# Optimization experiments

Measured on AMD Instinct MI355X. Metric: run time of the kernel, lower is better.

## Reference

```python
import jax, jax.numpy as jnp
import numpy as np

MAX_NORM = 20.0
V, D, B, L, K = 100000, 64, 4096, 50, 3


def setup_inputs() -> dict:
    key = jax.random.key(0)
    k0, k1, k2, k3 = jax.random.split(key, 4)
    embeddings = jax.random.normal(k0, (V, D), dtype=jnp.float32)
    tokens_l = jax.random.randint(k1, (B, L), 0, V)
    tokens_r = jax.random.randint(k2, (B, L), 0, V)
    tokens_neg = jax.random.randint(k3, (B, K, L), 0, V)
    return {"embeddings": embeddings, "tokens_l": tokens_l,
            "tokens_r": tokens_r, "tokens_neg": tokens_neg}


def _renorm(w):
    # nn.Embedding(max_norm=20): rows with norm > max_norm are rescaled to max_norm
    norms = jnp.linalg.norm(w, axis=1, keepdims=True)
    scale = jnp.where(norms > MAX_NORM, MAX_NORM / norms, 1.0)
    return w * scale


def _embed_bag(w, tokens):
    # gather rows then sum-pool over the last (token) axis -> embedding-bag 'sum'
    return jnp.take(w, tokens, axis=0).sum(axis=-2)


def reference(embeddings, tokens_l, tokens_r, tokens_neg):
    w = _renorm(embeddings)
    l_batch = _embed_bag(w, tokens_l)[:, None, :]     # [B, 1, D]
    r_batch = _embed_bag(w, tokens_r)[:, None, :]     # [B, 1, D]
    neg_batch = _embed_bag(w, tokens_neg)             # [B, K, D]
    return (l_batch, r_batch, neg_batch)
```

## Files before the change

### kernel.cpp

```cpp
#include <hip/hip_runtime.h>
#include <math.h>

#define V_SZ 100000
#define D_SZ 64
#define B_SZ 4096
#define L_SZ 50
#define K_SZ 3
#define MAX_NORM 20.0f

__global__ __launch_bounds__(256) void renorm_scale_kernel(
    const float* __restrict__ emb, float* __restrict__ scale) {
    int row = blockIdx.x * 16 + (threadIdx.x >> 4);
    int lane16 = threadIdx.x & 15;
    if (row >= V_SZ) return;
    const float4* row4 = (const float4*)(emb + (long)row * D_SZ);
    float4 v = row4[lane16];
    float ss = v.x * v.x + v.y * v.y + v.z * v.z + v.w * v.w;
    #pragma unroll
    for (int off = 8; off >= 1; off >>= 1)
        ss += __shfl_xor(ss, off, 16);
    if (lane16 == 0) {
        float n = sqrtf(ss);
        scale[row] = (n > MAX_NORM) ? (MAX_NORM / n) : 1.0f;
    }
}

__global__ __launch_bounds__(256) void embed_bag_kernel(
    const float* __restrict__ emb, const float* __restrict__ scale,
    const int* __restrict__ tl, const int* __restrict__ tr,
    const int* __restrict__ tn, float* __restrict__ out) {
    const int NBAGS = B_SZ * (2 + K_SZ);
    int wave = (int)((blockIdx.x * (unsigned)blockDim.x + threadIdx.x) >> 6);
    int lane = threadIdx.x & 63;
    if (wave >= NBAGS) return;

    const int* tok;
    if (wave < B_SZ)            tok = tl + (long)wave * L_SZ;
    else if (wave < 2 * B_SZ)   tok = tr + (long)(wave - B_SZ) * L_SZ;
    else                        tok = tn + (long)(wave - 2 * B_SZ) * L_SZ;

    int   t = (lane < L_SZ) ? tok[lane] : 0;
    float s = (lane < L_SZ) ? scale[t] : 0.0f;

    int m = lane & 15;
    int g = lane >> 4;

    float4 acc = make_float4(0.f, 0.f, 0.f, 0.f);
    #pragma unroll
    for (int i = 0; i < 13; ++i) {
        int j = i * 4 + g;
        int   tj = __shfl(t, j, 64);
        float sj = __shfl(s, j, 64);
        const float4* row = (const float4*)(emb + (long)tj * D_SZ);
        float4 v = row[m];
        acc.x = fmaf(sj, v.x, acc.x);
        acc.y = fmaf(sj, v.y, acc.y);
        acc.z = fmaf(sj, v.z, acc.z);
        acc.w = fmaf(sj, v.w, acc.w);
    }

    #pragma unroll
    for (int off = 16; off <= 32; off <<= 1) {
        acc.x += __shfl_xor(acc.x, off, 64);
        acc.y += __shfl_xor(acc.y, off, 64);
        acc.z += __shfl_xor(acc.z, off, 64);
        acc.w += __shfl_xor(acc.w, off, 64);
    }
    if (g == 0) {
        float4* o = (float4*)(out + (long)wave * D_SZ);
        o[m] = acc;
    }
}

extern "C" void kernel_launch(void* const* d_in, const int* in_sizes, int n_in,
                              void* d_out, int out_size, void* d_ws, size_t ws_size,
                              hipStream_t stream) {
    const float* emb = (const float*)d_in[0];
    const int* tl = (const int*)d_in[1];
    const int* tr = (const int*)d_in[2];
    const int* tn = (const int*)d_in[3];
    float* out = (float*)d_out;
    float* scale = (float*)d_ws;

    renorm_scale_kernel<<<(V_SZ + 15) / 16, 256, 0, stream>>>(emb, scale);

    const int NBAGS = B_SZ * (2 + K_SZ);
    int grid = NBAGS / 4;
    embed_bag_kernel<<<grid, 256, 0, stream>>>(emb, scale, tl, tr, tn, out);
}
```

Before: 110.7 us.

## Fuse row renorm into embedding-bag gather, drop separate scale kernel

Removes the separate kernel that computed a per-row scale over the whole vocabulary. Each gathered row's norm is now computed inline from the loaded float4 values with a 16-lane shuffle reduction. This avoids a full pass over the 25.6MB table and the scale-array gather, plus one launch. In exchange it adds shuffles and a sqrt per gathered row, and recomputes the norm for every duplicated token (about 1M gathers against 100K rows).

```diff
diff --git a/kernel.cpp b/kernel.cpp
--- a/kernel.cpp
+++ b/kernel.cpp
@@ -8,25 +8,8 @@
 #define K_SZ 3
 #define MAX_NORM 20.0f
 
-__global__ __launch_bounds__(256) void renorm_scale_kernel(
-    const float* __restrict__ emb, float* __restrict__ scale) {
-    int row = blockIdx.x * 16 + (threadIdx.x >> 4);
-    int lane16 = threadIdx.x & 15;
-    if (row >= V_SZ) return;
-    const float4* row4 = (const float4*)(emb + (long)row * D_SZ);
-    float4 v = row4[lane16];
-    float ss = v.x * v.x + v.y * v.y + v.z * v.z + v.w * v.w;
-    #pragma unroll
-    for (int off = 8; off >= 1; off >>= 1)
-        ss += __shfl_xor(ss, off, 16);
-    if (lane16 == 0) {
-        float n = sqrtf(ss);
-        scale[row] = (n > MAX_NORM) ? (MAX_NORM / n) : 1.0f;
-    }
-}
-
-__global__ __launch_bounds__(256) void embed_bag_kernel(
-    const float* __restrict__ emb, const float* __restrict__ scale,
+__global__ __launch_bounds__(256) void fused_bag_kernel(
+    const float* __restrict__ emb,
     const int* __restrict__ tl, const int* __restrict__ tr,
     const int* __restrict__ tn, float* __restrict__ out) {
     const int NBAGS = B_SZ * (2 + K_SZ);
@@ -39,24 +22,30 @@
     else if (wave < 2 * B_SZ)   tok = tr + (long)(wave - B_SZ) * L_SZ;
     else                        tok = tn + (long)(wave - 2 * B_SZ) * L_SZ;
 
-    int   t = (lane < L_SZ) ? tok[lane] : 0;
-    float s = (lane < L_SZ) ? scale[t] : 0.0f;
+    int t = (lane < L_SZ) ? tok[lane] : 0;
 
     int m = lane & 15;
     int g = lane >> 4;
 
     float4 acc = make_float4(0.f, 0.f, 0.f, 0.f);
+
     #pragma unroll
     for (int i = 0; i < 13; ++i) {
         int j = i * 4 + g;
-        int   tj = __shfl(t, j, 64);
-        float sj = __shfl(s, j, 64);
+        int tj = __shfl(t, j, 64);
         const float4* row = (const float4*)(emb + (long)tj * D_SZ);
         float4 v = row[m];
-        acc.x = fmaf(sj, v.x, acc.x);
-        acc.y = fmaf(sj, v.y, acc.y);
-        acc.z = fmaf(sj, v.z, acc.z);
-        acc.w = fmaf(sj, v.w, acc.w);
+        float ss = v.x * v.x + v.y * v.y + v.z * v.z + v.w * v.w;
+        #pragma unroll
+        for (int off = 1; off <= 8; off <<= 1)
+            ss += __shfl_xor(ss, off, 16);
+        float n = sqrtf(ss);
+        float s = (n > MAX_NORM) ? (MAX_NORM / n) : 1.0f;
+        s = (j < L_SZ) ? s : 0.0f;
+        acc.x = fmaf(s, v.x, acc.x);
+        acc.y = fmaf(s, v.y, acc.y);
+        acc.z = fmaf(s, v.z, acc.z);
+        acc.w = fmaf(s, v.w, acc.w);
     }
 
     #pragma unroll
@@ -80,11 +69,9 @@
     const int* tr = (const int*)d_in[2];
     const int* tn = (const int*)d_in[3];
     float* out = (float*)d_out;
-    float* scale = (float*)d_ws;
-
-    renorm_scale_kernel<<<(V_SZ + 15) / 16, 256, 0, stream>>>(emb, scale);
+    (void)d_ws; (void)ws_size;
 
     const int NBAGS = B_SZ * (2 + K_SZ);
     int grid = NBAGS / 4;
-    embed_bag_kernel<<<grid, 256, 0, stream>>>(emb, scale, tl, tr, tn, out);
+    fused_bag_kernel<<<grid, 256, 0, stream>>>(emb, tl, tr, tn, out);
 }
```

After: 104.4 us. 1.06x faster.
